# Kernel tuning notes

Measured on AMD Instinct MI355X. Metric: run time of the kernel, lower is better.

Reference implementation:

```python
import jax, jax.numpy as jnp
import numpy as np

E = 1024        # embedding_dim
H = 16          # num_heads
DR = 1          # downsample_rate
INT = E // DR   # internal_dim
HD = INT // H   # head dim
B, NQ, NK = 4, 2048, 2048


def setup_inputs() -> dict:
    key = jax.random.key(0)
    ks = jax.random.split(key, 11)
    s_in = 1.0 / np.sqrt(E)
    s_int = 1.0 / np.sqrt(INT)
    return {
        "q": jax.random.normal(ks[0], (B, NQ, E), jnp.float32),
        "k": jax.random.normal(ks[1], (B, NK, E), jnp.float32),
        "v": jax.random.normal(ks[2], (B, NK, E), jnp.float32),
        "wq": jax.random.normal(ks[3], (E, INT), jnp.float32) * s_in,
        "bq": jnp.zeros((INT,), jnp.float32),
        "wk": jax.random.normal(ks[4], (E, INT), jnp.float32) * s_in,
        "bk": jnp.zeros((INT,), jnp.float32),
        "wv": jax.random.normal(ks[5], (E, INT), jnp.float32) * s_in,
        "bv": jnp.zeros((INT,), jnp.float32),
        "wo": jax.random.normal(ks[6], (INT, E), jnp.float32) * s_int,
        "bo": jnp.zeros((E,), jnp.float32),
    }


def _heads(x):
    # (B, N, INT) -> (B, H, N, HD)
    b, n, c = x.shape
    return x.reshape(b, n, H, c // H).transpose(0, 2, 1, 3)


def reference(q, k, v, wq, bq, wk, bk, wv, bv, wo, bo):
    qh = _heads(q @ wq + bq)          # (B,H,NQ,HD)
    kh = _heads(k @ wk + bk)          # (B,H,NK,HD)
    vh = _heads(v @ wv + bv)          # (B,H,NK,HD)
    scale = 1.0 / np.sqrt(HD)
    attn = jnp.einsum('bhqd,bhkd->bhqk', qh, kh) * scale  # (B,H,NQ,NK)
    attn = jax.nn.softmax(attn, axis=-1)
    out = jnp.einsum('bhqk,bhkd->bhqd', attn, vh)          # (B,H,NQ,HD)
    out = out.transpose(0, 2, 1, 3).reshape(q.shape[0], qh.shape[2], INT)
    return out @ wo + bo
```

## Files before the change

### kernel.cpp

```cpp
#include <hip/hip_runtime.h>
#include <hip/hip_bf16.h>
#include <cstdint>
#include <cstddef>

typedef __bf16 bf16_t;
typedef __bf16 bf16x8 __attribute__((ext_vector_type(8)));
typedef float f32x4 __attribute__((ext_vector_type(4)));
typedef float f32x16 __attribute__((ext_vector_type(16)));
typedef uint32_t u32;

#define EDIM 1024
#define HH 16
#define HD 64
#define NSEQ 2048
#define QSCALE 0.18033688011f

__device__ __forceinline__ void async_copy16(const bf16_t* gsrc, bf16_t* lds_dst) {
    __builtin_amdgcn_global_load_lds(
        (const __attribute__((address_space(1))) uint32_t*)gsrc,
        (__attribute__((address_space(3))) uint32_t*)lds_dst,
        16, 0, 0);
}

__global__ void transpose_all(const float* __restrict__ w0, const float* __restrict__ w1,
                              const float* __restrict__ w2, const float* __restrict__ w3,
                              bf16_t* __restrict__ o0, bf16_t* __restrict__ o1,
                              bf16_t* __restrict__ o2, bf16_t* __restrict__ o3) {
    __shared__ bf16_t t[64][65];
    const float* in;
    bf16_t* out;
    switch (blockIdx.z) {
        case 0: in = w0; out = o0; break;
        case 1: in = w1; out = o1; break;
        case 2: in = w2; out = o2; break;
        default: in = w3; out = o3; break;
    }
    const int tid = threadIdx.x;
    const int kt = blockIdx.x, nt = blockIdx.y;
    #pragma unroll
    for (int i = 0; i < 16; i++) {
        int idx = i * 256 + tid;
        int r = idx >> 6, c = idx & 63;
        t[r][c] = (bf16_t)in[(size_t)(kt * 64 + r) * 1024 + nt * 64 + c];
    }
    __syncthreads();
    #pragma unroll
    for (int i = 0; i < 16; i++) {
        int idx = i * 256 + tid;
        int r = idx >> 6, c = idx & 63;
        out[(size_t)(nt * 64 + r) * 1024 + kt * 64 + c] = t[c][r];
    }
}

__global__ __launch_bounds__(256, 2)
void gemm_qkv(const float* __restrict__ Aq, const float* __restrict__ Ak,
              const float* __restrict__ Av,
              const bf16_t* __restrict__ Wq, const bf16_t* __restrict__ Wk,
              const bf16_t* __restrict__ Wv,
              const float* __restrict__ bq, const float* __restrict__ bk,
              const float* __restrict__ bv,
              bf16_t* __restrict__ Qh, bf16_t* __restrict__ Kh,
              bf16_t* __restrict__ Vt) {
    constexpr int BM = 128, BN = 128, BK = 64, K = 1024, NT = K / BK;
    __shared__ bf16_t Asm[2][BM * BK];
    __shared__ bf16_t Bsm[2][BN * BK];
    const int tid = threadIdx.x;
    const int wave = tid >> 6, lane = tid & 63;
    const int quad = lane >> 4, l15 = lane & 15;
    const int bx = blockIdx.x, by = blockIdx.y;
    const int mt = (by >> 3) * 8 + bx;
    const int n0 = (by & 7) * BN;
    const int wt = mt >> 6;
    const int m0 = (mt - wt * 64) * BM;
    const int wm = (wave & 1) * 64, wn = (wave >> 1) * 64;

    const float*  A    = wt == 0 ? Aq : (wt == 1 ? Ak : Av);
    const bf16_t* Bt   = wt == 0 ? Wq : (wt == 1 ? Wk : Wv);
    const float*  bias = wt == 0 ? bq : (wt == 1 ? bk : bv);
    bf16_t*       Cout = wt == 0 ? Qh : (wt == 1 ? Kh : Vt);
    const float oscale = wt == 0 ? QSCALE : 1.0f;

    f32x4 acc[4][4] = {};
    float4 ar[8];

    auto loadA = [&](int t) {
        const int k0 = t * BK;
        #pragma unroll
        for (int i = 0; i < 4; i++) {
            int s = i * 256 + tid;
            int row = s >> 3, kc = (s & 7) ^ (row & 7);
            const float* sp = A + (size_t)(m0 + row) * K + k0 + kc * 8;
            ar[2 * i]     = *(const float4*)sp;
            ar[2 * i + 1] = *(const float4*)(sp + 4);
        }
    };
    auto writeA = [&](int buf) {
        #pragma unroll
        for (int i = 0; i < 4; i++) {
            int s = i * 256 + tid;
            float4 x = ar[2 * i], y = ar[2 * i + 1];
            bf16x8 vv = {(bf16_t)x.x, (bf16_t)x.y, (bf16_t)x.z, (bf16_t)x.w,
                         (bf16_t)y.x, (bf16_t)y.y, (bf16_t)y.z, (bf16_t)y.w};
            *(bf16x8*)&Asm[buf][s * 8] = vv;
        }
    };
    auto stageB = [&](int t, int buf) {
        const int k0 = t * BK;
        #pragma unroll
        for (int i = 0; i < 4; i++) {
            int s = i * 256 + tid;
            int row = s >> 3, kc = (s & 7) ^ (row & 7);
            async_copy16(Bt + (size_t)(n0 + row) * K + k0 + kc * 8, &Bsm[buf][s * 8]);
        }
    };

    loadA(0);
    stageB(0, 0);
    writeA(0);
    stageB(1, 1);
    asm volatile("s_waitcnt vmcnt(4)" ::: "memory");
    loadA(1);
    asm volatile("s_waitcnt lgkmcnt(0)" ::: "memory");
    __builtin_amdgcn_s_barrier();
    __builtin_amdgcn_sched_barrier(0);

    for (int t = 0; t < NT; ++t) {
        const int buf = t & 1;
        bf16x8 af[2][4], bfr[2][4];
        #pragma unroll
        for (int ks = 0; ks < 2; ks++) {
            #pragma unroll
            for (int mi = 0; mi < 4; mi++) {
                int row = wm + mi * 16 + l15;
                int g = ks * 4 + quad;
                af[ks][mi] = *(const bf16x8*)&Asm[buf][row * BK + ((g ^ (row & 7)) * 8)];
            }
            #pragma unroll
            for (int ni = 0; ni < 4; ni++) {
                int row = wn + ni * 16 + l15;
                int g = ks * 4 + quad;
                bfr[ks][ni] = *(const bf16x8*)&Bsm[buf][row * BK + ((g ^ (row & 7)) * 8)];
            }
        }
        #pragma unroll
        for (int ks = 0; ks < 2; ks++)
            #pragma unroll
            for (int mi = 0; mi < 4; mi++)
                #pragma unroll
                for (int ni = 0; ni < 4; ni++)
                    acc[mi][ni] = __builtin_amdgcn_mfma_f32_16x16x32_bf16(
                        af[ks][mi], bfr[ks][ni], acc[mi][ni], 0, 0, 0);

        if (t + 1 < NT) {
            __builtin_amdgcn_s_barrier();
            __builtin_amdgcn_sched_barrier(0);
            writeA(buf ^ 1);
            if (t + 2 < NT) {
                stageB(t + 2, buf);
                asm volatile("s_waitcnt vmcnt(4)" ::: "memory");
                loadA(t + 2);
            } else {
                asm volatile("s_waitcnt vmcnt(0)" ::: "memory");
            }
            asm volatile("s_waitcnt lgkmcnt(0)" ::: "memory");
            __builtin_amdgcn_s_barrier();
            __builtin_amdgcn_sched_barrier(0);
        }
    }

    #pragma unroll
    for (int mi = 0; mi < 4; mi++) {
        #pragma unroll
        for (int ni = 0; ni < 4; ni++) {
            #pragma unroll
            for (int r = 0; r < 4; r++) {
                int m = m0 + wm + mi * 16 + quad * 4 + r;
                int nch = n0 + wn + ni * 16 + l15;
                float v = (acc[mi][ni][r] + bias[nch]) * oscale;
                int b = m >> 11, n = m & 2047;
                int h = nch >> 6, d = nch & 63;
                if (wt < 2)
                    Cout[(((size_t)(b * HH + h)) * NSEQ + n) * HD + d] = (bf16_t)v;
                else
                    Cout[(((size_t)(b * HH + h)) * HD + d) * NSEQ + n] = (bf16_t)v;
            }
        }
    }
}

__global__ __launch_bounds__(256, 2)
void gemm_out(const bf16_t* __restrict__ A, const bf16_t* __restrict__ Bt,
              const float* __restrict__ bias, float* __restrict__ C) {
    constexpr int BM = 128, BN = 128, BK = 64, K = 1024, N = 1024, NT = K / BK;
    __shared__ bf16_t Asm[2][BM * BK];
    __shared__ bf16_t Bsm[2][BN * BK];
    const int tid = threadIdx.x;
    const int wave = tid >> 6, lane = tid & 63;
    const int quad = lane >> 4, l15 = lane & 15;
    const int bx = blockIdx.x, by = blockIdx.y;
    const int n0 = (by & 7) * BN;
    const int m0 = ((by >> 3) * 8 + bx) * BM;
    const int wm = (wave & 1) * 64, wn = (wave >> 1) * 64;

    f32x4 acc[4][4] = {};

    auto stage = [&](int t, int buf) {
        const int k0 = t * BK;
        #pragma unroll
        for (int i = 0; i < 4; i++) {
            int s = i * 256 + tid;
            int row = s >> 3, kc = (s & 7) ^ (row & 7);
            async_copy16(A + (size_t)(m0 + row) * K + k0 + kc * 8, &Asm[buf][s * 8]);
        }
        #pragma unroll
        for (int i = 0; i < 4; i++) {
            int s = i * 256 + tid;
            int row = s >> 3, kc = (s & 7) ^ (row & 7);
            async_copy16(Bt + (size_t)(n0 + row) * K + k0 + kc * 8, &Bsm[buf][s * 8]);
        }
    };

    stage(0, 0);
    stage(1, 1);
    asm volatile("s_waitcnt vmcnt(8)" ::: "memory");
    __builtin_amdgcn_s_barrier();
    __builtin_amdgcn_sched_barrier(0);

    for (int t = 0; t < NT; ++t) {
        const int buf = t & 1;
        bf16x8 af[2][4], bfr[2][4];
        #pragma unroll
        for (int ks = 0; ks < 2; ks++) {
            #pragma unroll
            for (int mi = 0; mi < 4; mi++) {
                int row = wm + mi * 16 + l15;
                int g = ks * 4 + quad;
                af[ks][mi] = *(const bf16x8*)&Asm[buf][row * BK + ((g ^ (row & 7)) * 8)];
            }
            #pragma unroll
            for (int ni = 0; ni < 4; ni++) {
                int row = wn + ni * 16 + l15;
                int g = ks * 4 + quad;
                bfr[ks][ni] = *(const bf16x8*)&Bsm[buf][row * BK + ((g ^ (row & 7)) * 8)];
            }
        }
        #pragma unroll
        for (int ks = 0; ks < 2; ks++)
            #pragma unroll
            for (int mi = 0; mi < 4; mi++)
                #pragma unroll
                for (int ni = 0; ni < 4; ni++)
                    acc[mi][ni] = __builtin_amdgcn_mfma_f32_16x16x32_bf16(
                        af[ks][mi], bfr[ks][ni], acc[mi][ni], 0, 0, 0);

        if (t + 1 < NT) {
            __builtin_amdgcn_s_barrier();
            __builtin_amdgcn_sched_barrier(0);
            if (t + 2 < NT) {
                stage(t + 2, buf);
                asm volatile("s_waitcnt vmcnt(8)" ::: "memory");
            } else {
                asm volatile("s_waitcnt vmcnt(0)" ::: "memory");
            }
            asm volatile("s_waitcnt lgkmcnt(0)" ::: "memory");
            __builtin_amdgcn_s_barrier();
            __builtin_amdgcn_sched_barrier(0);
        }
    }

    #pragma unroll
    for (int mi = 0; mi < 4; mi++) {
        #pragma unroll
        for (int ni = 0; ni < 4; ni++) {
            #pragma unroll
            for (int r = 0; r < 4; r++) {
                int m = m0 + wm + mi * 16 + quad * 4 + r;
                int nch = n0 + wn + ni * 16 + l15;
                C[(size_t)m * N + nch] = acc[mi][ni][r] + bias[nch];
            }
        }
    }
}

union PW { u32 w[4]; bf16x8 v; };

__device__ __forceinline__ u32 pack_bf16(float lo, float hi) {
    union { bf16_t h[2]; u32 u; } x;
    x.h[0] = (bf16_t)lo;
    x.h[1] = (bf16_t)hi;
    return x.u;
}

__device__ __forceinline__ void half_swap(u32& a, u32& b) {
    auto r = __builtin_amdgcn_permlane32_swap(a, b, false, false);
    a = r[0];
    b = r[1];
}

__device__ __forceinline__ void softmax_pack(const f32x16 sa, float* lp,
                                             PW& f0, PW& f1) {
    float p[16];
    #pragma unroll
    for (int r = 0; r < 16; r++) {
        p[r] = __builtin_amdgcn_exp2f(sa[r]);
        lp[r & 3] += p[r];
    }
    u32 x0 = pack_bf16(p[0],  p[1]),  x1 = pack_bf16(p[2],  p[3]);
    u32 x2 = pack_bf16(p[4],  p[5]),  x3 = pack_bf16(p[6],  p[7]);
    u32 x4 = pack_bf16(p[8],  p[9]),  x5 = pack_bf16(p[10], p[11]);
    u32 x6 = pack_bf16(p[12], p[13]), x7 = pack_bf16(p[14], p[15]);
    half_swap(x0, x2); half_swap(x1, x3);
    half_swap(x4, x6); half_swap(x5, x7);
    f0.w[0] = x0; f0.w[1] = x1; f0.w[2] = x2; f0.w[3] = x3;
    f1.w[0] = x4; f1.w[1] = x5; f1.w[2] = x6; f1.w[3] = x7;
}

__global__ __launch_bounds__(256, 2)
void attn_kernel(const bf16_t* __restrict__ Qh, const bf16_t* __restrict__ Kh,
                 const bf16_t* __restrict__ Vt, bf16_t* __restrict__ out) {
    __shared__ bf16_t Ks[2][64 * 64];
    __shared__ bf16_t Vs[2][64 * 64];
    const int tid = threadIdx.x, wave = tid >> 6, lane = tid & 63;
    const int l31 = lane & 31, hi = lane >> 5;
    const int B = blockIdx.x;
    const int qt = (B >> 3) & 15;
    const int bh = (B >> 7) * 8 + (B & 7);
    const int b = bh >> 4, h = bh & 15;

    const bf16_t* kbase = Kh + (size_t)bh * NSEQ * HD;
    const bf16_t* vbase = Vt + (size_t)bh * HD * NSEQ;

    bf16x8 qf[4];
    {
        const bf16_t* qrow =
            Qh + ((size_t)bh * NSEQ + qt * 128 + wave * 32 + l31) * HD + hi * 8;
        #pragma unroll
        for (int s = 0; s < 4; s++) qf[s] = *(const bf16x8*)(qrow + s * 16);
    }

    const bf16_t *ks0, *ks1, *vs0, *vs1;
    {
        int r0 = tid >> 3, c0 = tid & 7;
        int s1 = tid + 256;
        int r1 = s1 >> 3, c1 = s1 & 7;
        ks0 = kbase + r0 * HD + (c0 ^ (r0 & 7)) * 8;
        ks1 = kbase + r1 * HD + (c1 ^ (r1 & 7)) * 8;
        vs0 = vbase + (size_t)r0 * NSEQ + (c0 ^ (r0 & 7)) * 8;
        vs1 = vbase + (size_t)r1 * NSEQ + (c1 ^ (r1 & 7)) * 8;
    }

    async_copy16(ks0, &Ks[0][tid * 8]);
    async_copy16(ks1, &Ks[0][(tid + 256) * 8]);
    async_copy16(vs0, &Vs[0][tid * 8]);
    async_copy16(vs1, &Vs[0][(tid + 256) * 8]);

    f32x16 oacc[2] = {};
    float lp[4] = {};

    for (int t = 0; t < 32; t++) {
        const int cur = t & 1;
        __syncthreads();

        if (t < 31) {
            ks0 += 64 * HD; ks1 += 64 * HD;
            vs0 += 64;      vs1 += 64;
            async_copy16(ks0, &Ks[cur ^ 1][tid * 8]);
            async_copy16(ks1, &Ks[cur ^ 1][(tid + 256) * 8]);
            async_copy16(vs0, &Vs[cur ^ 1][tid * 8]);
            async_copy16(vs1, &Vs[cur ^ 1][(tid + 256) * 8]);
        }

        const f32x16 zero = {};
        f32x16 sacc0, sacc1;
        {
            int g = hi;
            int row0 = l31, row1 = 32 + l31;
            bf16x8 ak0 = *(const bf16x8*)&Ks[cur][row0 * 64 + ((g ^ (row0 & 7)) * 8)];
            bf16x8 ak1 = *(const bf16x8*)&Ks[cur][row1 * 64 + ((g ^ (row1 & 7)) * 8)];
            __builtin_amdgcn_s_setprio(1);
            sacc0 = __builtin_amdgcn_mfma_f32_32x32x16_bf16(ak0, qf[0], zero, 0, 0, 0);
            sacc1 = __builtin_amdgcn_mfma_f32_32x32x16_bf16(ak1, qf[0], zero, 0, 0, 0);
            __builtin_amdgcn_s_setprio(0);
        }
        #pragma unroll
        for (int s = 1; s < 4; s++) {
            int g = s * 2 + hi;
            int row0 = l31;
            int row1 = 32 + l31;
            bf16x8 ak0 = *(const bf16x8*)&Ks[cur][row0 * 64 + ((g ^ (row0 & 7)) * 8)];
            bf16x8 ak1 = *(const bf16x8*)&Ks[cur][row1 * 64 + ((g ^ (row1 & 7)) * 8)];
            __builtin_amdgcn_s_setprio(1);
            sacc0 = __builtin_amdgcn_mfma_f32_32x32x16_bf16(ak0, qf[s], sacc0, 0, 0, 0);
            sacc1 = __builtin_amdgcn_mfma_f32_32x32x16_bf16(ak1, qf[s], sacc1, 0, 0, 0);
            __builtin_amdgcn_s_setprio(0);
        }

        PW pa[4];
        softmax_pack(sacc0, lp, pa[0], pa[1]);
        softmax_pack(sacc1, lp, pa[2], pa[3]);

        #pragma unroll
        for (int dt = 0; dt < 2; dt++) {
            #pragma unroll
            for (int ks = 0; ks < 4; ks++) {
                int row = dt * 32 + l31;
                int g = ks * 2 + hi;
                bf16x8 bv = *(const bf16x8*)&Vs[cur][row * 64 + ((g ^ (row & 7)) * 8)];
                __builtin_amdgcn_s_setprio(1);
                oacc[dt] = __builtin_amdgcn_mfma_f32_32x32x16_bf16(
                    pa[ks].v, bv, oacc[dt], 0, 0, 0);
                __builtin_amdgcn_s_setprio(0);
            }
        }
    }

    float lsum = (lp[0] + lp[1]) + (lp[2] + lp[3]);
    lsum += __shfl_xor(lsum, 32, 64);
    float linv = 1.f / lsum;
    float rinv[16];
    #pragma unroll
    for (int r = 0; r < 16; r++) {
        int q = (r & 3) + 8 * (r >> 2) + 4 * hi;
        rinv[r] = __shfl(linv, q, 64);
    }

    const int n0 = qt * 128 + wave * 32;
    #pragma unroll
    for (int dt = 0; dt < 2; dt++) {
        int c = h * 64 + dt * 32 + l31;
        #pragma unroll
        for (int r = 0; r < 16; r++) {
            int q = (r & 3) + 8 * (r >> 2) + 4 * hi;
            out[((size_t)b * NSEQ + n0 + q) * EDIM + c] = (bf16_t)(oacc[dt][r] * rinv[r]);
        }
    }
}

extern "C" void kernel_launch(void* const* d_in, const int* in_sizes, int n_in,
                              void* d_out, int out_size, void* d_ws, size_t ws_size,
                              hipStream_t stream) {
    const float* q  = (const float*)d_in[0];
    const float* k  = (const float*)d_in[1];
    const float* v  = (const float*)d_in[2];
    const float* wq = (const float*)d_in[3];
    const float* bq = (const float*)d_in[4];
    const float* wk = (const float*)d_in[5];
    const float* bk = (const float*)d_in[6];
    const float* wv = (const float*)d_in[7];
    const float* bv = (const float*)d_in[8];
    const float* wo = (const float*)d_in[9];
    const float* bo = (const float*)d_in[10];
    float* out = (float*)d_out;

    char* ws = (char*)d_ws;
    bf16_t* wqt = (bf16_t*)(ws + ((size_t)0  << 20));
    bf16_t* wkt = (bf16_t*)(ws + ((size_t)2  << 20));
    bf16_t* wvt = (bf16_t*)(ws + ((size_t)4  << 20));
    bf16_t* wot = (bf16_t*)(ws + ((size_t)6  << 20));

    bf16_t* Qh  = (bf16_t*)(ws + ((size_t)8  << 20));
    bf16_t* Kh  = (bf16_t*)(ws + ((size_t)24 << 20));
    bf16_t* Vt  = (bf16_t*)(ws + ((size_t)40 << 20));
    bf16_t* ao  = (bf16_t*)(ws + ((size_t)56 << 20));

    dim3 tb(256);

    transpose_all<<<dim3(16, 16, 4), tb, 0, stream>>>(wq, wk, wv, wo, wqt, wkt, wvt, wot);

    gemm_qkv<<<dim3(8, 192), tb, 0, stream>>>(q, k, v, wqt, wkt, wvt,
                                              bq, bk, bv, Qh, Kh, Vt);

    attn_kernel<<<1024, tb, 0, stream>>>(Qh, Kh, Vt, ao);

    gemm_out<<<dim3(8, 64), tb, 0, stream>>>(ao, wot, bo, out);
}
```

Measured before the change: 346.8 us.

## Enlarge projection GEMM tiles to 256x256 with 8 waves and XCD-aware block mapping

Measured after the change: 398.0 us. 1.15x slower.

```diff
diff --git a/kernel.cpp b/kernel.cpp
--- a/kernel.cpp
+++ b/kernel.cpp
@@ -20,6 +20,12 @@
         (const __attribute__((address_space(1))) uint32_t*)gsrc,
         (__attribute__((address_space(3))) uint32_t*)lds_dst,
         16, 0, 0);
+}
+
+__device__ __forceinline__ bf16x8 cvt8(float4 x, float4 y) {
+    bf16x8 v = {(bf16_t)x.x, (bf16_t)x.y, (bf16_t)x.z, (bf16_t)x.w,
+                (bf16_t)y.x, (bf16_t)y.y, (bf16_t)y.z, (bf16_t)y.w};
+    return v;
 }
 
 __global__ void transpose_all(const float* __restrict__ w0, const float* __restrict__ w1,
@@ -52,7 +58,7 @@
     }
 }
 
-__global__ __launch_bounds__(256, 2)
+__global__ __launch_bounds__(512, 2)
 void gemm_qkv(const float* __restrict__ Aq, const float* __restrict__ Ak,
               const float* __restrict__ Av,
               const bf16_t* __restrict__ Wq, const bf16_t* __restrict__ Wk,
@@ -61,18 +67,19 @@
               const float* __restrict__ bv,
               bf16_t* __restrict__ Qh, bf16_t* __restrict__ Kh,
               bf16_t* __restrict__ Vt) {
-    constexpr int BM = 128, BN = 128, BK = 64, K = 1024, NT = K / BK;
+    constexpr int BM = 256, BN = 256, BK = 64, K = 1024, NT = K / BK;
     __shared__ bf16_t Asm[2][BM * BK];
     __shared__ bf16_t Bsm[2][BN * BK];
     const int tid = threadIdx.x;
     const int wave = tid >> 6, lane = tid & 63;
     const int quad = lane >> 4, l15 = lane & 15;
-    const int bx = blockIdx.x, by = blockIdx.y;
-    const int mt = (by >> 3) * 8 + bx;
-    const int n0 = (by & 7) * BN;
-    const int wt = mt >> 6;
-    const int m0 = (mt - wt * 64) * BM;
-    const int wm = (wave & 1) * 64, wn = (wave >> 1) * 64;
+    const int id = blockIdx.y * 4 + blockIdx.x;
+    const int xcd = id & 7, j = id >> 3;
+    const int mt = xcd * 12 + (j >> 2);
+    const int n0 = (j & 3) * BN;
+    const int wt = mt >> 5;
+    const int m0 = (mt & 31) * BM;
+    const int wm = (wave & 1) * 128, wn = (wave >> 1) * 64;
 
     const float*  A    = wt == 0 ? Aq : (wt == 1 ? Ak : Av);
     const bf16_t* Bt   = wt == 0 ? Wq : (wt == 1 ? Wk : Wv);
@@ -80,14 +87,14 @@
     bf16_t*       Cout = wt == 0 ? Qh : (wt == 1 ? Kh : Vt);
     const float oscale = wt == 0 ? QSCALE : 1.0f;
 
-    f32x4 acc[4][4] = {};
+    f32x4 acc[8][4] = {};
     float4 ar[8];
 
     auto loadA = [&](int t) {
         const int k0 = t * BK;
         #pragma unroll
         for (int i = 0; i < 4; i++) {
-            int s = i * 256 + tid;
+            int s = i * 512 + tid;
             int row = s >> 3, kc = (s & 7) ^ (row & 7);
             const float* sp = A + (size_t)(m0 + row) * K + k0 + kc * 8;
             ar[2 * i]     = *(const float4*)sp;
@@ -97,18 +104,15 @@
     auto writeA = [&](int buf) {
         #pragma unroll
         for (int i = 0; i < 4; i++) {
-            int s = i * 256 + tid;
-            float4 x = ar[2 * i], y = ar[2 * i + 1];
-            bf16x8 vv = {(bf16_t)x.x, (bf16_t)x.y, (bf16_t)x.z, (bf16_t)x.w,
-                         (bf16_t)y.x, (bf16_t)y.y, (bf16_t)y.z, (bf16_t)y.w};
-            *(bf16x8*)&Asm[buf][s * 8] = vv;
+            int s = i * 512 + tid;
+            *(bf16x8*)&Asm[buf][s * 8] = cvt8(ar[2 * i], ar[2 * i + 1]);
         }
     };
     auto stageB = [&](int t, int buf) {
         const int k0 = t * BK;
         #pragma unroll
         for (int i = 0; i < 4; i++) {
-            int s = i * 256 + tid;
+            int s = i * 512 + tid;
             int row = s >> 3, kc = (s & 7) ^ (row & 7);
             async_copy16(Bt + (size_t)(n0 + row) * K + k0 + kc * 8, &Bsm[buf][s * 8]);
         }
@@ -126,30 +130,30 @@
 
     for (int t = 0; t < NT; ++t) {
         const int buf = t & 1;
-        bf16x8 af[2][4], bfr[2][4];
         #pragma unroll
         for (int ks = 0; ks < 2; ks++) {
-            #pragma unroll
-            for (int mi = 0; mi < 4; mi++) {
+            bf16x8 af[8], bfr[4];
+            #pragma unroll
+            for (int mi = 0; mi < 8; mi++) {
                 int row = wm + mi * 16 + l15;
                 int g = ks * 4 + quad;
-                af[ks][mi] = *(const bf16x8*)&Asm[buf][row * BK + ((g ^ (row & 7)) * 8)];
+                af[mi] = *(const bf16x8*)&Asm[buf][row * BK + ((g ^ (row & 7)) * 8)];
             }
             #pragma unroll
             for (int ni = 0; ni < 4; ni++) {
                 int row = wn + ni * 16 + l15;
                 int g = ks * 4 + quad;
-                bfr[ks][ni] = *(const bf16x8*)&Bsm[buf][row * BK + ((g ^ (row & 7)) * 8)];
-            }
-        }
-        #pragma unroll
-        for (int ks = 0; ks < 2; ks++)
-            #pragma unroll
-            for (int mi = 0; mi < 4; mi++)
+                bfr[ni] = *(const bf16x8*)&Bsm[buf][row * BK + ((g ^ (row & 7)) * 8)];
+            }
+            __builtin_amdgcn_s_setprio(1);
+            #pragma unroll
+            for (int mi = 0; mi < 8; mi++)
                 #pragma unroll
                 for (int ni = 0; ni < 4; ni++)
                     acc[mi][ni] = __builtin_amdgcn_mfma_f32_16x16x32_bf16(
-                        af[ks][mi], bfr[ks][ni], acc[mi][ni], 0, 0, 0);
+                        af[mi], bfr[ni], acc[mi][ni], 0, 0, 0);
+            __builtin_amdgcn_s_setprio(0);
+        }
 
         if (t + 1 < NT) {
             __builtin_amdgcn_s_barrier();
@@ -169,7 +173,7 @@
     }
 
     #pragma unroll
-    for (int mi = 0; mi < 4; mi++) {
+    for (int mi = 0; mi < 8; mi++) {
         #pragma unroll
         for (int ni = 0; ni < 4; ni++) {
             #pragma unroll
@@ -188,33 +192,35 @@
     }
 }
 
-__global__ __launch_bounds__(256, 2)
+__global__ __launch_bounds__(512, 2)
 void gemm_out(const bf16_t* __restrict__ A, const bf16_t* __restrict__ Bt,
               const float* __restrict__ bias, float* __restrict__ C) {
-    constexpr int BM = 128, BN = 128, BK = 64, K = 1024, N = 1024, NT = K / BK;
+    constexpr int BM = 256, BN = 256, BK = 64, K = 1024, N = 1024, NT = K / BK;
     __shared__ bf16_t Asm[2][BM * BK];
     __shared__ bf16_t Bsm[2][BN * BK];
     const int tid = threadIdx.x;
     const int wave = tid >> 6, lane = tid & 63;
     const int quad = lane >> 4, l15 = lane & 15;
-    const int bx = blockIdx.x, by = blockIdx.y;
-    const int n0 = (by & 7) * BN;
-    const int m0 = ((by >> 3) * 8 + bx) * BM;
-    const int wm = (wave & 1) * 64, wn = (wave >> 1) * 64;
-
-    f32x4 acc[4][4] = {};
+    const int id = blockIdx.y * 4 + blockIdx.x;
+    const int xcd = id & 7, j = id >> 3;
+    const int mt = xcd * 4 + (j >> 2);
+    const int n0 = (j & 3) * BN;
+    const int m0 = mt * BM;
+    const int wm = (wave & 1) * 128, wn = (wave >> 1) * 64;
+
+    f32x4 acc[8][4] = {};
 
     auto stage = [&](int t, int buf) {
         const int k0 = t * BK;
         #pragma unroll
         for (int i = 0; i < 4; i++) {
-            int s = i * 256 + tid;
+            int s = i * 512 + tid;
             int row = s >> 3, kc = (s & 7) ^ (row & 7);
             async_copy16(A + (size_t)(m0 + row) * K + k0 + kc * 8, &Asm[buf][s * 8]);
         }
         #pragma unroll
         for (int i = 0; i < 4; i++) {
-            int s = i * 256 + tid;
+            int s = i * 512 + tid;
             int row = s >> 3, kc = (s & 7) ^ (row & 7);
             async_copy16(Bt + (size_t)(n0 + row) * K + k0 + kc * 8, &Bsm[buf][s * 8]);
         }
@@ -228,30 +234,30 @@
 
     for (int t = 0; t < NT; ++t) {
         const int buf = t & 1;
-        bf16x8 af[2][4], bfr[2][4];
         #pragma unroll
         for (int ks = 0; ks < 2; ks++) {
-            #pragma unroll
-            for (int mi = 0; mi < 4; mi++) {
+            bf16x8 af[8], bfr[4];
+            #pragma unroll
+            for (int mi = 0; mi < 8; mi++) {
                 int row = wm + mi * 16 + l15;
                 int g = ks * 4 + quad;
-                af[ks][mi] = *(const bf16x8*)&Asm[buf][row * BK + ((g ^ (row & 7)) * 8)];
+                af[mi] = *(const bf16x8*)&Asm[buf][row * BK + ((g ^ (row & 7)) * 8)];
             }
             #pragma unroll
             for (int ni = 0; ni < 4; ni++) {
                 int row = wn + ni * 16 + l15;
                 int g = ks * 4 + quad;
-                bfr[ks][ni] = *(const bf16x8*)&Bsm[buf][row * BK + ((g ^ (row & 7)) * 8)];
-            }
-        }
-        #pragma unroll
-        for (int ks = 0; ks < 2; ks++)
-            #pragma unroll
-            for (int mi = 0; mi < 4; mi++)
+                bfr[ni] = *(const bf16x8*)&Bsm[buf][row * BK + ((g ^ (row & 7)) * 8)];
+            }
+            __builtin_amdgcn_s_setprio(1);
+            #pragma unroll
+            for (int mi = 0; mi < 8; mi++)
                 #pragma unroll
                 for (int ni = 0; ni < 4; ni++)
                     acc[mi][ni] = __builtin_amdgcn_mfma_f32_16x16x32_bf16(
-                        af[ks][mi], bfr[ks][ni], acc[mi][ni], 0, 0, 0);
+                        af[mi], bfr[ni], acc[mi][ni], 0, 0, 0);
+            __builtin_amdgcn_s_setprio(0);
+        }
 
         if (t + 1 < NT) {
             __builtin_amdgcn_s_barrier();
@@ -269,7 +275,7 @@
     }
 
     #pragma unroll
-    for (int mi = 0; mi < 4; mi++) {
+    for (int mi = 0; mi < 8; mi++) {
         #pragma unroll
         for (int ni = 0; ni < 4; ni++) {
             #pragma unroll
@@ -463,14 +469,13 @@
     bf16_t* Vt  = (bf16_t*)(ws + ((size_t)40 << 20));
     bf16_t* ao  = (bf16_t*)(ws + ((size_t)56 << 20));
 
-    dim3 tb(256);
-
-    transpose_all<<<dim3(16, 16, 4), tb, 0, stream>>>(wq, wk, wv, wo, wqt, wkt, wvt, wot);
-
-    gemm_qkv<<<dim3(8, 192), tb, 0, stream>>>(q, k, v, wqt, wkt, wvt,
-                                              bq, bk, bv, Qh, Kh, Vt);
-
-    attn_kernel<<<1024, tb, 0, stream>>>(Qh, Kh, Vt, ao);
-
-    gemm_out<<<dim3(8, 64), tb, 0, stream>>>(ao, wot, bo, out);
-}
+    transpose_all<<<dim3(16, 16, 4), dim3(256), 0, stream>>>(wq, wk, wv, wo,
+                                                             wqt, wkt, wvt, wot);
+
+    gemm_qkv<<<dim3(4, 96), dim3(512), 0, stream>>>(q, k, v, wqt, wkt, wvt,
+                                                    bq, bk, bv, Qh, Kh, Vt);
+
+    attn_kernel<<<1024, dim3(256), 0, stream>>>(Qh, Kh, Vt, ao);
+
+    gemm_out<<<dim3(4, 32), dim3(512), 0, stream>>>(ao, wot, bo, out);
+}
```
